# Performance work log

Measured on AMD Instinct MI355X. Metric: run time of the kernel, lower is better.

The kernel has to match this reference:

```python
import jax, jax.numpy as jnp
import numpy as np

B, S, D = 2, 2048, 512
H = 8
HD = D // H  # head dim = 64


def setup_inputs() -> dict:
    key = jax.random.key(0)
    ks = jax.random.split(key, 4)
    scale = 1.0 / np.sqrt(D)
    x = jax.random.normal(ks[0], (B, S, D), dtype=jnp.float32)
    wq = jax.random.normal(ks[1], (D, D), dtype=jnp.float32) * scale
    wk = jax.random.normal(ks[2], (D, D), dtype=jnp.float32) * scale
    wv = jax.random.normal(ks[3], (D, D), dtype=jnp.float32) * scale
    bq = jnp.zeros((D,), dtype=jnp.float32)
    bk = jnp.zeros((D,), dtype=jnp.float32)
    bv = jnp.zeros((D,), dtype=jnp.float32)
    return {"x": x, "wq": wq, "bq": bq, "wk": wk, "bk": bk, "wv": wv, "bv": bv}


def reference(x, wq, bq, wk, bk, wv, bv):
    # Linear projections (torch Linear: y = x @ W^T + b; weights here stored as [out,in])
    q = x @ wq.T + bq  # [B,S,D]
    k = x @ wk.T + bk
    v = x @ wv.T + bv
    # split heads -> [B,H,S,HD]
    q = q.reshape(B, S, H, HD).transpose(0, 2, 1, 3)
    k = k.reshape(B, S, H, HD).transpose(0, 2, 1, 3)
    v = v.reshape(B, S, H, HD).transpose(0, 2, 1, 3)
    # QK^T scores, scaled by 1/sqrt(head_dim)
    scores = jnp.einsum("bhqd,bhkd->bhqk", q, k) / jnp.sqrt(jnp.float32(HD))
    # softmax-free: elementwise sigmoid instead of softmax normalization
    attn = jax.nn.sigmoid(scores)  # [B,H,S,S] — the memory-bound intermediate
    out = jnp.einsum("bhqk,bhkd->bhqd", attn, v)
    # merge heads -> [B,S,D]
    return out.transpose(0, 2, 1, 3).reshape(B, S, D)
```

## Files before the change

### kernel.cpp

```cpp
#include <hip/hip_runtime.h>
#include <cstdint>
#include <cstddef>

#define BB   2
#define SS   2048
#define DD   512
#define HH   8
#define HDIM 64
#define XN   ((size_t)BB * SS * DD)
#define WN   ((size_t)DD * DD)

typedef __attribute__((ext_vector_type(8)))  short          s16x8;
typedef __attribute__((ext_vector_type(8)))  unsigned short u16x8;
typedef __attribute__((ext_vector_type(16))) float          f32x16;

static __device__ __forceinline__ unsigned short f2bf(float f) {
  union { float f; unsigned u; } x; x.f = f;
  unsigned r = x.u + 0x7fffu + ((x.u >> 16) & 1u);
  return (unsigned short)(r >> 16);
}
static __device__ __forceinline__ unsigned packtrunc(float lo, float hi) {
  return __builtin_amdgcn_perm(__float_as_uint(hi), __float_as_uint(lo), 0x07060302u);
}

#define QSCALE (-0.18033688011111543f)

__global__ __launch_bounds__(256) void cvtw_kernel(
    const float* __restrict__ wq, const float* __restrict__ wk, const float* __restrict__ wv,
    unsigned short* __restrict__ wb3) {
  const int z = blockIdx.y;
  const float* src = (z == 0) ? wq : (z == 1) ? wk : wv;
  unsigned short* dst = wb3 + (size_t)z * WN;
  int i = (blockIdx.x * 256 + threadIdx.x) * 4;
  float4 f = *(const float4*)(src + i);
  ushort4 o;
  o.x = f2bf(f.x); o.y = f2bf(f.y); o.z = f2bf(f.z); o.w = f2bf(f.w);
  *(ushort4*)(dst + i) = o;
}

__global__ __launch_bounds__(256, 1) void proj_kernel(
    const float* __restrict__ x, const unsigned short* __restrict__ wb3,
    const float* __restrict__ bq, const float* __restrict__ bk, const float* __restrict__ bv,
    unsigned short* __restrict__ qo, unsigned short* __restrict__ ko,
    unsigned short* __restrict__ vt) {
  __shared__ unsigned short As[2][128 * 40];
  __shared__ unsigned short Bs[2][3][64 * 40];

  const int t = threadIdx.x;
  const int lane = t & 63, wave = t >> 6;
  const int ln = lane & 31, hi = lane >> 5;
  const int m0 = blockIdx.x * 128, n0 = blockIdx.y * 64;

  float4 axf[2][2];
  u16x8 br[3];
#pragma unroll
  for (int i = 0; i < 2; i++) {
    int c = t + i * 256;
    const float* ap = x + (size_t)(m0 + (c >> 2)) * DD + (c & 3) * 8;
    axf[i][0] = *(const float4*)ap;
    axf[i][1] = *(const float4*)(ap + 4);
  }
#pragma unroll
  for (int z = 0; z < 3; z++)
    br[z] = *(const u16x8*)&wb3[(size_t)z * WN + (size_t)(n0 + (t >> 2)) * DD + (t & 3) * 8];

#pragma unroll
  for (int i = 0; i < 2; i++) {
    int c = t + i * 256;
    u16x8 ar;
#pragma unroll
    for (int j = 0; j < 4; j++) {
      ar[j]     = f2bf(((const float*)&axf[i][0])[j]);
      ar[4 + j] = f2bf(((const float*)&axf[i][1])[j]);
    }
    *(u16x8*)&As[0][(c >> 2) * 40 + (c & 3) * 8] = ar;
  }
#pragma unroll
  for (int z = 0; z < 3; z++)
    *(u16x8*)&Bs[0][z][(t >> 2) * 40 + (t & 3) * 8] = br[z];
  __syncthreads();

  f32x16 acc[3][2];
#pragma unroll
  for (int z = 0; z < 3; z++) { acc[z][0] = (f32x16){}; acc[z][1] = (f32x16){}; }

#pragma unroll 2
  for (int kt = 0; kt < 16; kt++) {
    const int cur = kt & 1, nxt = cur ^ 1;
    if (kt < 15) {
      int k0 = (kt + 1) * 32;
#pragma unroll
      for (int i = 0; i < 2; i++) {
        int c = t + i * 256;
        const float* ap = x + (size_t)(m0 + (c >> 2)) * DD + k0 + (c & 3) * 8;
        axf[i][0] = *(const float4*)ap;
        axf[i][1] = *(const float4*)(ap + 4);
      }
#pragma unroll
      for (int z = 0; z < 3; z++)
        br[z] = *(const u16x8*)&wb3[(size_t)z * WN + (size_t)(n0 + (t >> 2)) * DD + k0 + (t & 3) * 8];
    }
#pragma unroll
    for (int cc = 0; cc < 2; cc++) {
      s16x8 af = *(const s16x8*)&As[cur][(wave * 32 + ln) * 40 + cc * 16 + hi * 8];
#pragma unroll
      for (int z = 0; z < 3; z++) {
        s16x8 b0 = *(const s16x8*)&Bs[cur][z][(ln) * 40 + cc * 16 + hi * 8];
        s16x8 b1 = *(const s16x8*)&Bs[cur][z][(32 + ln) * 40 + cc * 16 + hi * 8];
        acc[z][0] = __builtin_amdgcn_mfma_f32_32x32x16_bf16(af, b0, acc[z][0], 0, 0, 0);
        acc[z][1] = __builtin_amdgcn_mfma_f32_32x32x16_bf16(af, b1, acc[z][1], 0, 0, 0);
      }
    }
    if (kt < 15) {
#pragma unroll
      for (int i = 0; i < 2; i++) {
        int c = t + i * 256;
        u16x8 ar;
#pragma unroll
        for (int j = 0; j < 4; j++) {
          ar[j]     = f2bf(((const float*)&axf[i][0])[j]);
          ar[4 + j] = f2bf(((const float*)&axf[i][1])[j]);
        }
        *(u16x8*)&As[nxt][(c >> 2) * 40 + (c & 3) * 8] = ar;
      }
#pragma unroll
      for (int z = 0; z < 3; z++)
        *(u16x8*)&Bs[nxt][z][(t >> 2) * 40 + (t & 3) * 8] = br[z];
    }
    __syncthreads();
  }

  const int h = blockIdx.y;
  const int bidx = m0 >> 11;
  const int sbase = (m0 & 2047) + wave * 32;
  const size_t bhb = (size_t)(bidx * HH + h) * SS * HDIM;
  const int kts = sbase >> 5;

#pragma unroll
  for (int nh = 0; nh < 2; nh++) {
    const int hd = nh * 32 + ln;
    {
      f32x16 av = acc[0][nh];
      const float bval = bq[n0 + hd];
#pragma unroll
      for (int r = 0; r < 16; r++) {
        int s = sbase + (r & 3) + 8 * (r >> 2) + 4 * hi;
        qo[bhb + (size_t)s * HDIM + hd] = f2bf((av[r] + bval) * QSCALE);
      }
    }
    {
      f32x16 av = acc[1][nh];
      const float bval = bk[n0 + hd];
      const int c = hd >> 4, hk = (hd >> 3) & 1, j = hd & 7;
      unsigned short* kd = ko + bhb + ((size_t)kts * 4 + c) * 512 + j;
#pragma unroll
      for (int r = 0; r < 16; r++) {
        int off = (r & 3) + 8 * (r >> 2) + 4 * hi;
        kd[(hk * 32 + off) * 8] = f2bf(av[r] + bval);
      }
    }
    {
      f32x16 av = acc[2][nh];
      const float bval = bv[n0 + hd];
      unsigned short* vd = vt + bhb + ((size_t)kts * 4 + nh * 2) * 512 + hi * 256 + ln * 8;
#pragma unroll
      for (int g = 0; g < 4; g++) {
        unsigned short* vg = vd + (g >> 1) * 512 + (g & 1) * 4;
#pragma unroll
        for (int j2 = 0; j2 < 4; j2 += 2) {
          unsigned pk = (unsigned)f2bf(av[g * 4 + j2] + bval) |
                        ((unsigned)f2bf(av[g * 4 + j2 + 1] + bval) << 16);
          *(unsigned*)&vg[j2] = pk;
        }
      }
    }
  }
}

__global__ __launch_bounds__(512, 2) void attn_kernel(
    const unsigned short* __restrict__ qb,
    const unsigned short* __restrict__ kfb,
    const unsigned short* __restrict__ vfb,
    float* __restrict__ out) {
  __shared__ __align__(16) float red[2 * 8192];

  const int t = threadIdx.x;
  const int lane = t & 63, wave = t >> 6;
  const int ln = lane & 31, hi = lane >> 5;
  const int qp = wave & 1, kh = wave >> 1;
  const int fid = blockIdx.y * 16 + blockIdx.x;
  const int bh = fid & 15, qx = fid >> 4;
  const int b = bh >> 3, h = bh & 7;
  const unsigned short* qp_ = qb + (size_t)bh * SS * HDIM;
  const unsigned short* kfp = kfb + (size_t)bh * SS * HDIM;
  const unsigned short* vfp = vfb + (size_t)bh * SS * HDIM;
  const int q0 = qx * 128 + qp * 64;

  s16x8 qf[2][4];
#pragma unroll
  for (int qs = 0; qs < 2; qs++)
#pragma unroll
    for (int c = 0; c < 4; c++)
      qf[qs][c] = *(const s16x8*)&qp_[(size_t)(q0 + qs * 32 + ln) * HDIM + c * 16 + hi * 8];

  f32x16 o00 = {}, o01 = {}, o10 = {}, o11 = {};

  s16x8 kf[4], vf[4];
  int foff = kh * 16 * 2048 + lane * 8;
#pragma unroll
  for (int c = 0; c < 4; c++) {
    kf[c] = *(const s16x8*)&kfp[foff + c * 512];
    vf[c] = *(const s16x8*)&vfp[foff + c * 512];
  }
  foff += 2048;

#pragma unroll 1
  for (int i = 0; i < 16; i++) {
    f32x16 st0 = {}, st1 = {};
#pragma unroll
    for (int c = 0; c < 4; c++) {
      st0 = __builtin_amdgcn_mfma_f32_32x32x16_bf16(kf[c], qf[0][c], st0, 0, 0, 0);
      st1 = __builtin_amdgcn_mfma_f32_32x32x16_bf16(kf[c], qf[1][c], st1, 0, 0, 0);
    }

    if (i < 15) {
#pragma unroll
      for (int c = 0; c < 4; c++)
        kf[c] = *(const s16x8*)&kfp[foff + c * 512];
    }

    unsigned pg[2][8];
#pragma unroll
    for (int qs = 0; qs < 2; qs++) {
      f32x16 st = qs ? st1 : st0;
#pragma unroll
      for (int g = 0; g < 4; g++) {
        float p0 = __builtin_amdgcn_rcpf(1.0f + __builtin_amdgcn_exp2f(st[4 * g + 0]));
        float p1 = __builtin_amdgcn_rcpf(1.0f + __builtin_amdgcn_exp2f(st[4 * g + 1]));
        float p2 = __builtin_amdgcn_rcpf(1.0f + __builtin_amdgcn_exp2f(st[4 * g + 2]));
        float p3 = __builtin_amdgcn_rcpf(1.0f + __builtin_amdgcn_exp2f(st[4 * g + 3]));
        pg[qs][2 * g]     = packtrunc(p0, p1);
        pg[qs][2 * g + 1] = packtrunc(p2, p3);
      }
    }

#pragma unroll
    for (int c = 0; c < 2; c++) {
#pragma unroll
      for (int qs = 0; qs < 2; qs++) {
        union { unsigned u[4]; s16x8 v; } pu;
        pu.u[0] = pg[qs][4 * c + 0];
        pu.u[1] = pg[qs][4 * c + 1];
        pu.u[2] = pg[qs][4 * c + 2];
        pu.u[3] = pg[qs][4 * c + 3];
        if (qs == 0) {
          o00 = __builtin_amdgcn_mfma_f32_32x32x16_bf16(pu.v, vf[c], o00, 0, 0, 0);
          o01 = __builtin_amdgcn_mfma_f32_32x32x16_bf16(pu.v, vf[2 + c], o01, 0, 0, 0);
        } else {
          o10 = __builtin_amdgcn_mfma_f32_32x32x16_bf16(pu.v, vf[c], o10, 0, 0, 0);
          o11 = __builtin_amdgcn_mfma_f32_32x32x16_bf16(pu.v, vf[2 + c], o11, 0, 0, 0);
        }
      }
    }

    if (i < 15) {
#pragma unroll
      for (int c = 0; c < 4; c++)
        vf[c] = *(const s16x8*)&vfp[foff + c * 512];
      foff += 2048;
    }
  }

  if (kh >= 2) {
    float* slot = red + (kh - 2) * 8192;
#pragma unroll
    for (int qs = 0; qs < 2; qs++)
#pragma unroll
      for (int dh = 0; dh < 2; dh++) {
        f32x16 ov = qs ? (dh ? o11 : o10) : (dh ? o01 : o00);
#pragma unroll
        for (int r = 0; r < 16; r++) {
          int ql = qp * 64 + qs * 32 + (r & 3) + 8 * (r >> 2) + 4 * hi;
          slot[ql * 64 + dh * 32 + ln] = ov[r];
        }
      }
  }
  __syncthreads();
  if (kh < 2) {
    float* slot = red + kh * 8192;
#pragma unroll
    for (int qs = 0; qs < 2; qs++)
#pragma unroll
      for (int dh = 0; dh < 2; dh++) {
        f32x16 ov = qs ? (dh ? o11 : o10) : (dh ? o01 : o00);
#pragma unroll
        for (int r = 0; r < 16; r++) {
          int ql = qp * 64 + qs * 32 + (r & 3) + 8 * (r >> 2) + 4 * hi;
          slot[ql * 64 + dh * 32 + ln] += ov[r];
        }
      }
  }
  __syncthreads();
  const float4* r0 = (const float4*)red;
  const float4* r1 = (const float4*)(red + 8192);
  const int qblk = qx * 128;
#pragma unroll
  for (int j = 0; j < 4; j++) {
    int g = t + j * 512;
    float4 s0 = r0[g], s1 = r1[g];
    float4 s;
    s.x = s0.x + s1.x; s.y = s0.y + s1.y; s.z = s0.z + s1.z; s.w = s0.w + s1.w;
    int q = g >> 4, dbase = (g & 15) * 4;
    *(float4*)&out[((size_t)(b * SS + qblk + q)) * DD + h * HDIM + dbase] = s;
  }
}

extern "C" void kernel_launch(void* const* d_in, const int* in_sizes, int n_in,
                              void* d_out, int out_size, void* d_ws, size_t ws_size,
                              hipStream_t stream) {
  const float* x  = (const float*)d_in[0];
  const float* wq = (const float*)d_in[1];
  const float* bq = (const float*)d_in[2];
  const float* wk = (const float*)d_in[3];
  const float* bk = (const float*)d_in[4];
  const float* wv = (const float*)d_in[5];
  const float* bv = (const float*)d_in[6];
  float* out = (float*)d_out;

  unsigned short* wb = (unsigned short*)d_ws;
  unsigned short* qo = wb + 3 * WN;
  unsigned short* ko = qo + XN;
  unsigned short* vt = ko + XN;

  cvtw_kernel<<<dim3(256, 3), 256, 0, stream>>>(wq, wk, wv, wb);
  proj_kernel<<<dim3(32, 8), 256, 0, stream>>>(x, wb, bq, bk, bv, qo, ko, vt);
  attn_kernel<<<dim3(SS / 128, BB * HH), 512, 0, stream>>>(qo, ko, vt, out);
}
```

Baseline: 113.4 us.

## Pre-swizzle weights into MFMA fragment layout and drop LDS staging in projection

The weight conversion kernel now writes bf16 weights in a fragment-ordered layout, so each lane of the projection kernel can load its MFMA B operand directly from global memory. The projection GEMM no longer stages A and B tiles through shared memory or synchronises with barriers. Each wave instead loads its own x rows and weight fragments straight into registers, using a two-deep register prefetch. This removes LDS traffic and block-wide syncs, but the four waves now each fetch the same weight fragments redundantly, and the x loads are less coalesced.

```diff
diff --git a/kernel.cpp b/kernel.cpp
--- a/kernel.cpp
+++ b/kernel.cpp
@@ -33,104 +33,69 @@
   unsigned short* dst = wb3 + (size_t)z * WN;
   int i = (blockIdx.x * 256 + threadIdx.x) * 4;
   float4 f = *(const float4*)(src + i);
+  int n = i >> 9, k = i & 511;
+  int off = (n >> 6) * 32768 + (k >> 4) * 1024 + ((n >> 5) & 1) * 512 +
+            (n & 31) * 16 + ((k >> 3) & 1) * 8 + (k & 7);
   ushort4 o;
   o.x = f2bf(f.x); o.y = f2bf(f.y); o.z = f2bf(f.z); o.w = f2bf(f.w);
-  *(ushort4*)(dst + i) = o;
+  *(ushort4*)&dst[off] = o;
 }
 
 __global__ __launch_bounds__(256, 1) void proj_kernel(
-    const float* __restrict__ x, const unsigned short* __restrict__ wb3,
+    const float* __restrict__ x, const unsigned short* __restrict__ wfrag,
     const float* __restrict__ bq, const float* __restrict__ bk, const float* __restrict__ bv,
     unsigned short* __restrict__ qo, unsigned short* __restrict__ ko,
     unsigned short* __restrict__ vt) {
-  __shared__ unsigned short As[2][128 * 40];
-  __shared__ unsigned short Bs[2][3][64 * 40];
-
   const int t = threadIdx.x;
   const int lane = t & 63, wave = t >> 6;
   const int ln = lane & 31, hi = lane >> 5;
-  const int m0 = blockIdx.x * 128, n0 = blockIdx.y * 64;
-
-  float4 axf[2][2];
-  u16x8 br[3];
-#pragma unroll
-  for (int i = 0; i < 2; i++) {
-    int c = t + i * 256;
-    const float* ap = x + (size_t)(m0 + (c >> 2)) * DD + (c & 3) * 8;
-    axf[i][0] = *(const float4*)ap;
-    axf[i][1] = *(const float4*)(ap + 4);
-  }
-#pragma unroll
-  for (int z = 0; z < 3; z++)
-    br[z] = *(const u16x8*)&wb3[(size_t)z * WN + (size_t)(n0 + (t >> 2)) * DD + (t & 3) * 8];
-
-#pragma unroll
-  for (int i = 0; i < 2; i++) {
-    int c = t + i * 256;
-    u16x8 ar;
+  const int m0 = blockIdx.x * 128;
+  const int h = blockIdx.y;
+  const int n0 = h * 64;
+
+  const float* xp = x + (size_t)(m0 + wave * 32 + ln) * DD + hi * 8;
+  const unsigned short* wp = wfrag + h * 32768 + ln * 16 + hi * 8;
+
+  float4 a4[2][2];
+  s16x8 bfr[2][3][2];
+#pragma unroll
+  for (int s = 0; s < 2; s++) {
+    a4[s][0] = *(const float4*)(xp + s * 16);
+    a4[s][1] = *(const float4*)(xp + s * 16 + 4);
+#pragma unroll
+    for (int z = 0; z < 3; z++)
+#pragma unroll
+      for (int nh = 0; nh < 2; nh++)
+        bfr[s][z][nh] = *(const s16x8*)&wp[z * (int)WN + s * 1024 + nh * 512];
+  }
+
+  f32x16 acc[3][2] = {};
+
+#pragma unroll 2
+  for (int s = 0; s < 32; s++) {
+    const int cur = s & 1;
+    s16x8 af;
 #pragma unroll
     for (int j = 0; j < 4; j++) {
-      ar[j]     = f2bf(((const float*)&axf[i][0])[j]);
-      ar[4 + j] = f2bf(((const float*)&axf[i][1])[j]);
-    }
-    *(u16x8*)&As[0][(c >> 2) * 40 + (c & 3) * 8] = ar;
-  }
-#pragma unroll
-  for (int z = 0; z < 3; z++)
-    *(u16x8*)&Bs[0][z][(t >> 2) * 40 + (t & 3) * 8] = br[z];
-  __syncthreads();
-
-  f32x16 acc[3][2];
-#pragma unroll
-  for (int z = 0; z < 3; z++) { acc[z][0] = (f32x16){}; acc[z][1] = (f32x16){}; }
-
-#pragma unroll 2
-  for (int kt = 0; kt < 16; kt++) {
-    const int cur = kt & 1, nxt = cur ^ 1;
-    if (kt < 15) {
-      int k0 = (kt + 1) * 32;
-#pragma unroll
-      for (int i = 0; i < 2; i++) {
-        int c = t + i * 256;
-        const float* ap = x + (size_t)(m0 + (c >> 2)) * DD + k0 + (c & 3) * 8;
-        axf[i][0] = *(const float4*)ap;
-        axf[i][1] = *(const float4*)(ap + 4);
-      }
+      af[j]     = (short)f2bf(((const float*)&a4[cur][0])[j]);
+      af[4 + j] = (short)f2bf(((const float*)&a4[cur][1])[j]);
+    }
+#pragma unroll
+    for (int z = 0; z < 3; z++)
+#pragma unroll
+      for (int nh = 0; nh < 2; nh++)
+        acc[z][nh] = __builtin_amdgcn_mfma_f32_32x32x16_bf16(af, bfr[cur][z][nh], acc[z][nh], 0, 0, 0);
+    if (s < 30) {
+      a4[cur][0] = *(const float4*)(xp + (s + 2) * 16);
+      a4[cur][1] = *(const float4*)(xp + (s + 2) * 16 + 4);
 #pragma unroll
       for (int z = 0; z < 3; z++)
-        br[z] = *(const u16x8*)&wb3[(size_t)z * WN + (size_t)(n0 + (t >> 2)) * DD + k0 + (t & 3) * 8];
-    }
-#pragma unroll
-    for (int cc = 0; cc < 2; cc++) {
-      s16x8 af = *(const s16x8*)&As[cur][(wave * 32 + ln) * 40 + cc * 16 + hi * 8];
-#pragma unroll
-      for (int z = 0; z < 3; z++) {
-        s16x8 b0 = *(const s16x8*)&Bs[cur][z][(ln) * 40 + cc * 16 + hi * 8];
-        s16x8 b1 = *(const s16x8*)&Bs[cur][z][(32 + ln) * 40 + cc * 16 + hi * 8];
-        acc[z][0] = __builtin_amdgcn_mfma_f32_32x32x16_bf16(af, b0, acc[z][0], 0, 0, 0);
-        acc[z][1] = __builtin_amdgcn_mfma_f32_32x32x16_bf16(af, b1, acc[z][1], 0, 0, 0);
-      }
-    }
-    if (kt < 15) {
-#pragma unroll
-      for (int i = 0; i < 2; i++) {
-        int c = t + i * 256;
-        u16x8 ar;
-#pragma unroll
-        for (int j = 0; j < 4; j++) {
-          ar[j]     = f2bf(((const float*)&axf[i][0])[j]);
-          ar[4 + j] = f2bf(((const float*)&axf[i][1])[j]);
-        }
-        *(u16x8*)&As[nxt][(c >> 2) * 40 + (c & 3) * 8] = ar;
-      }
-#pragma unroll
-      for (int z = 0; z < 3; z++)
-        *(u16x8*)&Bs[nxt][z][(t >> 2) * 40 + (t & 3) * 8] = br[z];
-    }
-    __syncthreads();
-  }
-
-  const int h = blockIdx.y;
+#pragma unroll
+        for (int nh = 0; nh < 2; nh++)
+          bfr[cur][z][nh] = *(const s16x8*)&wp[z * (int)WN + (s + 2) * 1024 + nh * 512];
+    }
+  }
+
   const int bidx = m0 >> 11;
   const int sbase = (m0 & 2047) + wave * 32;
   const size_t bhb = (size_t)(bidx * HH + h) * SS * HDIM;
```

Result: no change. 113.3 us (-0.1%).
